# Performance work log

Hardware: AMD Instinct MI355X
Metric: run time of the kernel (lower is better)

Reference implementation:

```python
import jax, jax.numpy as jnp
import numpy as np

DIM = 512
NUM_HEADS = 8
HEAD_DIM = DIM // NUM_HEADS
EPS = 1e-6


def setup_inputs() -> dict:
    key = jax.random.key(0)
    k_x, k_qkv, k_out, k_b = jax.random.split(key, 4)
    B, N = 8, 4096
    x = jax.random.normal(k_x, (B, N, DIM), dtype=jnp.float32)
    # nn.Linear weights stored as [out_features, in_features]; we keep [in, out] for x @ W
    s_qkv = 1.0 / np.sqrt(DIM)
    W_qkv = jax.random.uniform(k_qkv, (DIM, 3 * DIM), minval=-s_qkv, maxval=s_qkv, dtype=jnp.float32)
    W_out = jax.random.uniform(k_out, (DIM, DIM), minval=-s_qkv, maxval=s_qkv, dtype=jnp.float32)
    b_out = jax.random.uniform(k_b, (DIM,), minval=-s_qkv, maxval=s_qkv, dtype=jnp.float32)
    return {"x": x, "W_qkv": W_qkv, "W_out": W_out, "b_out": b_out}


def _feature_map(x):
    # elu(x) + 1
    return jax.nn.elu(x) + 1.0


def reference(x, W_qkv, W_out, b_out):
    B, N, C = x.shape
    H, D = NUM_HEADS, HEAD_DIM
    qkv = x @ W_qkv                              # [B, N, 3C]
    qkv = qkv.reshape(B, N, 3, H, D).transpose(2, 0, 3, 1, 4)  # [3, B, H, N, D]
    q, k, v = qkv[0], qkv[1], qkv[2]
    q_phi = _feature_map(q)                      # [B, H, N, D]
    k_phi = _feature_map(k)
    KV = jnp.einsum('bhnd,bhne->bhde', k_phi, v)  # [B, H, D, D]
    K_sum = k_phi.sum(axis=2)                     # [B, H, D]
    denom = jnp.einsum('bhnd,bhd->bhn', q_phi, K_sum)[..., None] + EPS  # [B, H, N, 1]
    out = jnp.einsum('bhnd,bhde->bhne', q_phi, KV) / denom              # [B, H, N, D]
    out = out.transpose(0, 2, 1, 3).reshape(B, N, C)
    return out @ W_out + b_out
```

## Files before the change

### kernel.cpp

```cpp
#include <hip/hip_runtime.h>
#include <stdint.h>

typedef float    f32x4 __attribute__((ext_vector_type(4)));
typedef short    s16x8 __attribute__((ext_vector_type(8)));
typedef short    s16x4 __attribute__((ext_vector_type(4)));
typedef unsigned short u16;
typedef uint32_t u32;

#define DEVINL __device__ __forceinline__

DEVINL float bf2f(u16 u) { union { u32 i; float f; } x; x.i = ((u32)u) << 16; return x.f; }
DEVINL u16 f2bf(float f) {
  union { float f; u32 i; } x; x.f = f;
  u32 i = x.i;
  return (u16)((i + 0x7FFFu + ((i >> 16) & 1u)) >> 16);
}

DEVINL void gload16(const void* g, void* l) {
  __builtin_amdgcn_global_load_lds((const __attribute__((address_space(1))) void*)g,
                                   (__attribute__((address_space(3))) void*)l,
                                   16, 0, 0);
}

__global__ __launch_bounds__(256) void k_prep(const float* __restrict__ x,
                                              u16* __restrict__ xb,
                                              const float* __restrict__ Wqkv,
                                              u16* __restrict__ wqkvt,
                                              const float* __restrict__ Wout,
                                              u16* __restrict__ woutt) {
  __shared__ __align__(16) float t[64][65];
  int b = blockIdx.x;
  int tid = threadIdx.x;
  if (b < 2048) {
    const int n8 = 2097152;
    int stride = 2048 * 256;
    for (int i = b * 256 + tid; i < n8; i += stride) {
      const f32x4* p = (const f32x4*)(x + (size_t)i * 8);
      f32x4 a = p[0], c = p[1];
      s16x8 o;
      o[0] = (short)f2bf(a[0]); o[1] = (short)f2bf(a[1]);
      o[2] = (short)f2bf(a[2]); o[3] = (short)f2bf(a[3]);
      o[4] = (short)f2bf(c[0]); o[5] = (short)f2bf(c[1]);
      o[6] = (short)f2bf(c[2]); o[7] = (short)f2bf(c[3]);
      *(s16x8*)(xb + (size_t)i * 8) = o;
    }
    return;
  }
  const float* W; u16* Wt; int K, N, tb;
  if (b < 2048 + 192) { W = Wqkv; Wt = wqkvt; K = 512; N = 1536; tb = b - 2048; }
  else               { W = Wout; Wt = woutt; K = 512; N = 512;  tb = b - 2240; }
  int nb = N >> 6;
  int tn = tb % nb, tk = tb / nb;
  int n0 = tn << 6, k0 = tk << 6;
  int cr = tid >> 4, cc = (tid & 15) << 2;
#pragma unroll
  for (int i = 0; i < 4; i++) {
    int r = cr + (i << 4);
    f32x4 v = *(const f32x4*)(W + (size_t)(k0 + r) * N + n0 + cc);
    t[r][cc] = v[0]; t[r][cc + 1] = v[1]; t[r][cc + 2] = v[2]; t[r][cc + 3] = v[3];
  }
  __syncthreads();
#pragma unroll
  for (int i = 0; i < 4; i++) {
    int nn = cr + (i << 4);
    s16x4 o;
    o[0] = (short)f2bf(t[cc    ][nn]);
    o[1] = (short)f2bf(t[cc + 1][nn]);
    o[2] = (short)f2bf(t[cc + 2][nn]);
    o[3] = (short)f2bf(t[cc + 3][nn]);
    *(s16x4*)(Wt + (size_t)(n0 + nn) * K + k0 + cc) = o;
  }
}

__global__ __launch_bounds__(256, 2) void k_g1(
    const u16* __restrict__ A, const u16* __restrict__ Bt,
    u16* __restrict__ qph, u16* __restrict__ kphT, u16* __restrict__ vT) {
  __shared__ __align__(16) u16 lsA[3][128 * 32];
  __shared__ __align__(16) u16 lsB[3][256 * 32];
  const int nbn = 6;
  int nwg = gridDim.x, bx = blockIdx.x;
  int o = (bx & 7) * (nwg >> 3) + (bx >> 3);
  int bm = o / nbn, bn = o % nbn;
  int m0 = bm << 7, n0 = bn << 8;
  int tid = threadIdx.x, w = tid >> 6, lane = tid & 63;
  int lnlo = lane & 15, lnhi = lane >> 4;

  if ((bx >> 8) & 1) __builtin_amdgcn_s_sleep(30);

  const u16* gAp[2]; int lda[2];
#pragma unroll
  for (int i = 0; i < 2; i++) {
    int c = tid + i * 256, row = c >> 2, ch = c & 3;
    gAp[i] = A + (size_t)(m0 + row) * 512 + (ch ^ ((row >> 1) & 3)) * 8;
    lda[i] = c * 8;
  }
  const u16* gBp[4]; int ldb[4];
#pragma unroll
  for (int i = 0; i < 4; i++) {
    int c = tid + i * 256, row = c >> 2, ch = c & 3;
    gBp[i] = Bt + (size_t)(n0 + row) * 512 + (ch ^ ((row >> 1) & 3)) * 8;
    ldb[i] = c * 8;
  }
  int offA[8], offB[4];
#pragma unroll
  for (int f = 0; f < 8; f++) { int r = f * 16 + lnlo;          offA[f] = r * 32 + (lnhi ^ ((r >> 1) & 3)) * 8; }
#pragma unroll
  for (int f = 0; f < 4; f++) { int r = w * 64 + f * 16 + lnlo; offB[f] = r * 32 + (lnhi ^ ((r >> 1) & 3)) * 8; }

  f32x4 acc[8][4] = {};

#pragma unroll
  for (int tt = 0; tt < 2; tt++) {
#pragma unroll
    for (int i = 0; i < 2; i++) gload16(gAp[i] + tt * 32, &lsA[tt][lda[i]]);
#pragma unroll
    for (int i = 0; i < 4; i++) gload16(gBp[i] + tt * 32, &lsB[tt][ldb[i]]);
  }
  asm volatile("s_waitcnt vmcnt(6)" ::: "memory");
  __builtin_amdgcn_s_barrier();

#pragma unroll
  for (int t = 0; t < 16; t++) {
    int buf = t % 3;
    const u16* La = &lsA[buf][0];
    const u16* Lb = &lsB[buf][0];
    int k2 = (t + 2) * 32, b2 = (t + 2) % 3;

    s16x8 bf[4], af[4];
#pragma unroll
    for (int f = 0; f < 4; f++) bf[f] = *(const s16x8*)(Lb + offB[f]);
#pragma unroll
    for (int f = 0; f < 4; f++) af[f] = *(const s16x8*)(La + offA[f]);
    if (t < 14) {
#pragma unroll
      for (int i = 0; i < 2; i++) gload16(gAp[i] + k2, &lsA[b2][lda[i]]);
    }
    __builtin_amdgcn_s_barrier();
    __builtin_amdgcn_s_setprio(1);
#pragma unroll
    for (int mf = 0; mf < 4; mf++)
#pragma unroll
      for (int nf = 0; nf < 4; nf++)
        acc[mf][nf] = __builtin_amdgcn_mfma_f32_16x16x32_bf16(af[mf], bf[nf], acc[mf][nf], 0, 0, 0);
    __builtin_amdgcn_s_setprio(0);
    __builtin_amdgcn_s_barrier();

    s16x8 af2[4];
#pragma unroll
    for (int f = 0; f < 4; f++) af2[f] = *(const s16x8*)(La + offA[4 + f]);
    if (t < 14) {
#pragma unroll
      for (int i = 0; i < 4; i++) gload16(gBp[i] + k2, &lsB[b2][ldb[i]]);
    }
    __builtin_amdgcn_s_barrier();
    __builtin_amdgcn_s_setprio(1);
#pragma unroll
    for (int mf = 0; mf < 4; mf++)
#pragma unroll
      for (int nf = 0; nf < 4; nf++)
        acc[4 + mf][nf] = __builtin_amdgcn_mfma_f32_16x16x32_bf16(af2[mf], bf[nf], acc[4 + mf][nf], 0, 0, 0);
    __builtin_amdgcn_s_setprio(0);
    if (t <= 13)      asm volatile("s_waitcnt vmcnt(6)" ::: "memory");
    else if (t == 14) asm volatile("s_waitcnt vmcnt(0)" ::: "memory");
    if (t < 15) __builtin_amdgcn_s_barrier();
  }

  int gnB = n0 + w * 64;
  int sec = n0 >> 9;
  if (sec == 0) {
#pragma unroll
    for (int mf = 0; mf < 8; mf++) {
#pragma unroll
      for (int nf = 0; nf < 4; nf++) {
        int col = gnB + nf * 16 + lnlo;
        int hh = (col >> 6) & 7;
        int dd = col & 63;
#pragma unroll
        for (int r = 0; r < 4; r++) {
          int rowm = m0 + mf * 16 + lnhi * 4 + r;
          float val = acc[mf][nf][r];
          val = (val > 0.f) ? (val + 1.f) : __expf(val);
          int bidx = rowm >> 12, tok = rowm & 4095;
          qph[(((size_t)(bidx * 8 + hh) * 4096 + tok) << 6) + dd] = f2bf(val);
        }
      }
    }
  } else {
    u16* dstT = (sec == 1) ? kphT : vT;
    bool isphi = (sec == 1);
#pragma unroll
    for (int mf = 0; mf < 8; mf++) {
      int rowm = m0 + mf * 16 + lnhi * 4;
      int bidx = rowm >> 12, tok = rowm & 4095;
#pragma unroll
      for (int nf = 0; nf < 4; nf++) {
        int col = gnB + nf * 16 + lnlo;
        int hh = (col >> 6) & 7;
        int dd = col & 63;
        s16x4 o4;
#pragma unroll
        for (int r = 0; r < 4; r++) {
          float val = acc[mf][nf][r];
          if (isphi) val = (val > 0.f) ? (val + 1.f) : __expf(val);
          o4[r] = (short)f2bf(val);
        }
        *(s16x4*)&dstT[((size_t)(bidx * 8 + hh) * 64 + dd) * 4096 + tok] = o4;
      }
    }
  }
}

template <int EPI>
__global__ __launch_bounds__(512, 1) void k_gemm(
    const u16* __restrict__ A, const u16* __restrict__ Bt,
    int nbn,
    u16* __restrict__ qph, u16* __restrict__ kphT, u16* __restrict__ vT,
    float* __restrict__ out, const float* __restrict__ bias) {
  __shared__ __align__(16) u16 lsA[3][256 * 32];
  __shared__ __align__(16) u16 lsB[3][256 * 32];

  int nwg = gridDim.x;
  int bx = blockIdx.x;
  int o = (bx & 7) * (nwg >> 3) + (bx >> 3);
  int bm = o / nbn, bn = o % nbn;
  int m0 = bm << 8, n0 = bn << 8;
  int tid = threadIdx.x;
  int w = tid >> 6, lane = tid & 63;
  int lnlo = lane & 15, lnhi = lane >> 4;
  int wr = w >> 2, wc = w & 3;

  const u16* gAp[2]; const u16* gBp[2]; int ldst[2];
#pragma unroll
  for (int i = 0; i < 2; i++) {
    int c = tid + i * 512;
    int row = c >> 2, ch = c & 3;
    int gch = ch ^ ((row >> 1) & 3);
    gAp[i] = A + (size_t)(m0 + row) * 512 + gch * 8;
    gBp[i] = Bt + (size_t)(n0 + row) * 512 + gch * 8;
    ldst[i] = c * 8;
  }

  int offA[8], offB[4];
#pragma unroll
  for (int f = 0; f < 8; f++) {
    int r = wr * 128 + f * 16 + lnlo;
    offA[f] = r * 32 + (lnhi ^ ((r >> 1) & 3)) * 8;
  }
#pragma unroll
  for (int f = 0; f < 4; f++) {
    int r = wc * 64 + f * 16 + lnlo;
    offB[f] = r * 32 + (lnhi ^ ((r >> 1) & 3)) * 8;
  }

  f32x4 acc[8][4] = {};

#pragma unroll
  for (int i = 0; i < 2; i++) gload16(gAp[i], &lsA[0][ldst[i]]);
#pragma unroll
  for (int i = 0; i < 2; i++) gload16(gBp[i], &lsB[0][ldst[i]]);
#pragma unroll
  for (int i = 0; i < 2; i++) gload16(gAp[i] + 32, &lsA[1][ldst[i]]);
#pragma unroll
  for (int i = 0; i < 2; i++) gload16(gBp[i] + 32, &lsB[1][ldst[i]]);
  asm volatile("s_waitcnt vmcnt(4)" ::: "memory");
  __builtin_amdgcn_s_barrier();

#pragma unroll
  for (int t = 0; t < 16; t++) {
    int buf = t % 3;
    const u16* La = &lsA[buf][0];
    const u16* Lb = &lsB[buf][0];
    int k2 = (t + 2) * 32;
    int b2 = (t + 2) % 3;

    s16x8 bf[4], af[4];
#pragma unroll
    for (int f = 0; f < 4; f++) bf[f] = *(const s16x8*)(Lb + offB[f]);
#pragma unroll
    for (int f = 0; f < 4; f++) af[f] = *(const s16x8*)(La + offA[f]);
    if (t < 14) {
#pragma unroll
      for (int i = 0; i < 2; i++) gload16(gAp[i] + k2, &lsA[b2][ldst[i]]);
    }
    __builtin_amdgcn_s_barrier();
    __builtin_amdgcn_s_setprio(1);
#pragma unroll
    for (int mf = 0; mf < 4; mf++)
#pragma unroll
      for (int nf = 0; nf < 4; nf++)
        acc[mf][nf] = __builtin_amdgcn_mfma_f32_16x16x32_bf16(af[mf], bf[nf], acc[mf][nf], 0, 0, 0);
    __builtin_amdgcn_s_setprio(0);
    __builtin_amdgcn_s_barrier();

    s16x8 af2[4];
#pragma unroll
    for (int f = 0; f < 4; f++) af2[f] = *(const s16x8*)(La + offA[4 + f]);
    if (t < 14) {
#pragma unroll
      for (int i = 0; i < 2; i++) gload16(gBp[i] + k2, &lsB[b2][ldst[i]]);
    }
    __builtin_amdgcn_s_barrier();
    __builtin_amdgcn_s_setprio(1);
#pragma unroll
    for (int mf = 0; mf < 4; mf++)
#pragma unroll
      for (int nf = 0; nf < 4; nf++)
        acc[4 + mf][nf] = __builtin_amdgcn_mfma_f32_16x16x32_bf16(af2[mf], bf[nf], acc[4 + mf][nf], 0, 0, 0);
    __builtin_amdgcn_s_setprio(0);
    if (t <= 13)      asm volatile("s_waitcnt vmcnt(4)" ::: "memory");
    else if (t == 14) asm volatile("s_waitcnt vmcnt(0)" ::: "memory");
    if (t < 15) __builtin_amdgcn_s_barrier();
  }

  int gmB = m0 + wr * 128;
  int gnB = n0 + wc * 64;
#pragma unroll
  for (int mf = 0; mf < 8; mf++) {
#pragma unroll
    for (int nf = 0; nf < 4; nf++) {
      int col = gnB + nf * 16 + lnlo;
      float bv = bias[col];
#pragma unroll
      for (int r = 0; r < 4; r++) {
        int rowm = gmB + mf * 16 + lnhi * 4 + r;
        out[(size_t)rowm * 512 + col] = acc[mf][nf][r] + bv;
      }
    }
  }
}

__global__ __launch_bounds__(256, 2) void k_kv(const u16* __restrict__ kphT,
                                               const u16* __restrict__ vT,
                                               float* __restrict__ kvpart,
                                               float* __restrict__ kspart) {
  __shared__ __align__(16) u16 lsK[64 * 256];
  __shared__ __align__(16) u16 lsV[64 * 256];
  __shared__ float red[4][64];
  int bx = blockIdx.x;
  int bh = bx >> 4, ck = bx & 15;
  int tid = threadIdx.x, w = tid >> 6, lane = tid & 63;
  int lnlo = lane & 15, lnhi = lane >> 4;
  size_t gbase = (size_t)bh * 64 * 4096 + ck * 256;

#pragma unroll
  for (int i = 0; i < 8; i++) {
    int c = tid + i * 256;
    int row = c >> 5, ch = c & 31;
    int gch = ch ^ (row & 31);
    gload16(kphT + gbase + (size_t)row * 4096 + gch * 8, &lsK[c * 8]);
  }
#pragma unroll
  for (int i = 0; i < 8; i++) {
    int c = tid + i * 256;
    int row = c >> 5, ch = c & 31;
    int gch = ch ^ (row & 31);
    gload16(vT + gbase + (size_t)row * 4096 + gch * 8, &lsV[c * 8]);
  }
  asm volatile("s_waitcnt vmcnt(0)" ::: "memory");
  __builtin_amdgcn_s_barrier();

  f32x4 acc[4] = {{0.f, 0.f, 0.f, 0.f}, {0.f, 0.f, 0.f, 0.f},
                  {0.f, 0.f, 0.f, 0.f}, {0.f, 0.f, 0.f, 0.f}};
  int rb = w * 16 + lnlo;
#pragma unroll
  for (int kk = 0; kk < 8; kk++) {
    s16x8 bfr = *(const s16x8*)&lsV[rb * 256 + ((kk * 4 + lnhi) ^ (rb & 31)) * 8];
#pragma unroll
    for (int mf = 0; mf < 4; mf++) {
      int ra = mf * 16 + lnlo;
      s16x8 af = *(const s16x8*)&lsK[ra * 256 + ((kk * 4 + lnhi) ^ (ra & 31)) * 8];
      acc[mf] = __builtin_amdgcn_mfma_f32_16x16x32_bf16(af, bfr, acc[mf], 0, 0, 0);
    }
  }

  {
    int d = tid & 63, q = tid >> 6;
    float s = 0.f;
#pragma unroll
    for (int j = 0; j < 8; j++) {
      s16x8 v8 = *(const s16x8*)&lsK[d * 256 + (q * 8 + j) * 8];
#pragma unroll
      for (int e = 0; e < 8; e++) s += bf2f((u16)v8[e]);
    }
    red[q][d] = s;
  }
  __syncthreads();

  size_t pb = (size_t)(bh * 16 + ck) * 4096;
#pragma unroll
  for (int mf = 0; mf < 4; mf++)
#pragma unroll
    for (int r = 0; r < 4; r++)
      kvpart[pb + (size_t)(mf * 16 + lnhi * 4 + r) * 64 + (w * 16 + lnlo)] = acc[mf][r];
  if (tid < 64)
    kspart[(size_t)(bh * 16 + ck) * 64 + tid] =
        red[0][tid] + red[1][tid] + red[2][tid] + red[3][tid];
}

__global__ __launch_bounds__(256) void k_kvred(const float* __restrict__ kvpart,
                                               const float* __restrict__ kspart,
                                               u16* __restrict__ kvt_sw,
                                               float* __restrict__ ksum) {
  int bh = blockIdx.x;
  int tid = threadIdx.x;
  int e = tid >> 2, d0 = (tid & 3) * 16;
  size_t pb = (size_t)bh * 16 * 4096;
#pragma unroll
  for (int dd = 0; dd < 16; dd++) {
    int d = d0 + dd;
    float s = 0.f;
#pragma unroll
    for (int c = 0; c < 16; c++) s += kvpart[pb + (size_t)c * 4096 + d * 64 + e];
    int chs = (d >> 3) ^ (e & 7);
    kvt_sw[((size_t)bh * 64 + e) * 64 + chs * 8 + (d & 7)] = f2bf(s);
  }
  if (tid < 64) {
    float s = 0.f;
#pragma unroll
    for (int c = 0; c < 16; c++) s += kspart[(size_t)bh * 1024 + c * 64 + tid];
    ksum[bh * 64 + tid] = s;
  }
}

__global__ __launch_bounds__(256, 2) void k_attnout(const u16* __restrict__ qphi,
                                                    const u16* __restrict__ kvt_sw,
                                                    const float* __restrict__ ksum,
                                                    u16* __restrict__ y) {
  __shared__ __align__(16) u16 qa[256 * 64];
  __shared__ __align__(16) u16 bb[64 * 64];
  __shared__ float ksl[64];
  __shared__ float rdnl[256];
  int bx = blockIdx.x;
  int bh = bx >> 4, tch = bx & 15;
  int b = bh >> 3, hh = bh & 7;
  int tid = threadIdx.x, w = tid >> 6, lane = tid & 63;
  int lnlo = lane & 15, lnhi = lane >> 4;
  size_t qbase = ((size_t)bh * 4096 + tch * 256) * 64;

#pragma unroll
  for (int i = 0; i < 8; i++) {
    int c = i * 256 + tid;
    int row = c >> 3, ch = c & 7;
    int gcol = (ch ^ (row & 7)) << 3;
    gload16(qphi + qbase + (size_t)row * 64 + gcol, &qa[c * 8]);
  }
#pragma unroll
  for (int i = 0; i < 2; i++) {
    int c = i * 256 + tid;
    gload16(kvt_sw + (size_t)bh * 4096 + c * 8, &bb[c * 8]);
  }
  if (tid < 64) ksl[tid] = ksum[bh * 64 + tid];
  __syncthreads();

  {
    float den = 0.f;
#pragma unroll
    for (int ch = 0; ch < 8; ch++) {
      s16x8 v8 = *(const s16x8*)&qa[tid * 64 + ((ch ^ (tid & 7)) << 3)];
#pragma unroll
      for (int j = 0; j < 8; j++) den += bf2f((u16)v8[j]) * ksl[ch * 8 + j];
    }
    rdnl[tid] = 1.f / (den + 1e-6f);
  }
  __syncthreads();

  f32x4 acc[4][4] = {};
#pragma unroll
  for (int kk = 0; kk < 2; kk++) {
    s16x8 af[4], bfr[4];
#pragma unroll
    for (int f = 0; f < 4; f++) {
      int ra = w * 64 + f * 16 + lnlo;
      int ca = (kk * 4 + lnhi) ^ (ra & 7);
      af[f] = *(const s16x8*)&qa[ra * 64 + ca * 8];
      int rb = f * 16 + lnlo;
      int cb = (kk * 4 + lnhi) ^ (rb & 7);
      bfr[f] = *(const s16x8*)&bb[rb * 64 + cb * 8];
    }
#pragma unroll
    for (int mf = 0; mf < 4; mf++)
#pragma unroll
      for (int nf = 0; nf < 4; nf++)
        acc[mf][nf] = __builtin_amdgcn_mfma_f32_16x16x32_bf16(af[mf], bfr[nf], acc[mf][nf], 0, 0, 0);
  }

  size_t yrow0 = (size_t)b * 4096 + tch * 256;
#pragma unroll
  for (int mf = 0; mf < 4; mf++) {
#pragma unroll
    for (int nf = 0; nf < 4; nf++) {
      int e = nf * 16 + lnlo;
#pragma unroll
      for (int r = 0; r < 4; r++) {
        int tl = w * 64 + mf * 16 + lnhi * 4 + r;
        float val = acc[mf][nf][r] * rdnl[tl];
        y[(yrow0 + tl) * 512 + hh * 64 + e] = f2bf(val);
      }
    }
  }
}

#define OFF_XB     ((size_t)0)
#define OFF_WQKVT  ((size_t)33554432)
#define OFF_WOUTT  ((size_t)35127296)
#define OFF_QPHI   ((size_t)35651584)
#define OFF_KPHI   ((size_t)69206016)
#define OFF_VBUF   ((size_t)102760448)
#define OFF_KVPART ((size_t)136314880)
#define OFF_KSPART ((size_t)153092096)
#define OFF_KVT    ((size_t)153354240)
#define OFF_KSUM   ((size_t)153878528)

extern "C" void kernel_launch(void* const* d_in, const int* in_sizes, int n_in,
                              void* d_out, int out_size, void* d_ws, size_t ws_size,
                              hipStream_t stream) {
  const float* x    = (const float*)d_in[0];
  const float* Wqkv = (const float*)d_in[1];
  const float* Wout = (const float*)d_in[2];
  const float* bout = (const float*)d_in[3];
  float* out = (float*)d_out;
  char* ws = (char*)d_ws;

  u16* xb     = (u16*)(ws + OFF_XB);
  u16* y      = (u16*)(ws + OFF_XB);
  u16* wqkvt  = (u16*)(ws + OFF_WQKVT);
  u16* woutt  = (u16*)(ws + OFF_WOUTT);
  u16* qphi   = (u16*)(ws + OFF_QPHI);
  u16* kphT   = (u16*)(ws + OFF_KPHI);
  u16* vT     = (u16*)(ws + OFF_VBUF);
  float* kvpart = (float*)(ws + OFF_KVPART);
  float* kspart = (float*)(ws + OFF_KSPART);
  u16* kvt_sw = (u16*)(ws + OFF_KVT);
  float* ksum = (float*)(ws + OFF_KSUM);

  k_prep<<<2304, 256, 0, stream>>>(x, xb, Wqkv, wqkvt, Wout, woutt);

  k_g1<<<1536, 256, 0, stream>>>(xb, wqkvt, qphi, kphT, vT);
  k_kv<<<64 * 16, 256, 0, stream>>>(kphT, vT, kvpart, kspart);
  k_kvred<<<64, 256, 0, stream>>>(kvpart, kspart, kvt_sw, ksum);
  k_attnout<<<64 * 16, 256, 0, stream>>>(qphi, kvt_sw, ksum, y);
  k_gemm<1><<<256, 512, 0, stream>>>(y, woutt, 2, nullptr, nullptr, nullptr, out, bout);
}
```

Measured before the change: 160.8 us.

## Fold KV into output projection per batch and fuse attention-out into final GEMM

Precomputes per-batch W2 = blockdiag(KV_h) · W_out so the output becomes (q_phi scaled by 1/denom) @ W2 + bias. The separate attention-out kernel, its bf16 intermediate y, and the KV reduce kernel are removed, and the row normalization is applied while staging A tiles into LDS in the final GEMM. The QKV GEMM also moves from the 128x256 tile with 256 threads to the 256x256 tile with 512 threads. In exchange there is an extra small GEMM per batch and head to build W2, the A tiles go through registers instead of direct-to-LDS loads, and there is an extra bf16 rounding of W2.

Measured after the change: 153.6 us (median of 2 runs). 4.5% less time.

```diff
diff --git a/kernel.cpp b/kernel.cpp
--- a/kernel.cpp
+++ b/kernel.cpp
@@ -72,153 +72,12 @@
   }
 }
 
-__global__ __launch_bounds__(256, 2) void k_g1(
+__global__ __launch_bounds__(512, 1) void k_gemm1(
     const u16* __restrict__ A, const u16* __restrict__ Bt,
     u16* __restrict__ qph, u16* __restrict__ kphT, u16* __restrict__ vT) {
-  __shared__ __align__(16) u16 lsA[3][128 * 32];
+  __shared__ __align__(16) u16 lsA[3][256 * 32];
   __shared__ __align__(16) u16 lsB[3][256 * 32];
   const int nbn = 6;
-  int nwg = gridDim.x, bx = blockIdx.x;
-  int o = (bx & 7) * (nwg >> 3) + (bx >> 3);
-  int bm = o / nbn, bn = o % nbn;
-  int m0 = bm << 7, n0 = bn << 8;
-  int tid = threadIdx.x, w = tid >> 6, lane = tid & 63;
-  int lnlo = lane & 15, lnhi = lane >> 4;
-
-  if ((bx >> 8) & 1) __builtin_amdgcn_s_sleep(30);
-
-  const u16* gAp[2]; int lda[2];
-#pragma unroll
-  for (int i = 0; i < 2; i++) {
-    int c = tid + i * 256, row = c >> 2, ch = c & 3;
-    gAp[i] = A + (size_t)(m0 + row) * 512 + (ch ^ ((row >> 1) & 3)) * 8;
-    lda[i] = c * 8;
-  }
-  const u16* gBp[4]; int ldb[4];
-#pragma unroll
-  for (int i = 0; i < 4; i++) {
-    int c = tid + i * 256, row = c >> 2, ch = c & 3;
-    gBp[i] = Bt + (size_t)(n0 + row) * 512 + (ch ^ ((row >> 1) & 3)) * 8;
-    ldb[i] = c * 8;
-  }
-  int offA[8], offB[4];
-#pragma unroll
-  for (int f = 0; f < 8; f++) { int r = f * 16 + lnlo;          offA[f] = r * 32 + (lnhi ^ ((r >> 1) & 3)) * 8; }
-#pragma unroll
-  for (int f = 0; f < 4; f++) { int r = w * 64 + f * 16 + lnlo; offB[f] = r * 32 + (lnhi ^ ((r >> 1) & 3)) * 8; }
-
-  f32x4 acc[8][4] = {};
-
-#pragma unroll
-  for (int tt = 0; tt < 2; tt++) {
-#pragma unroll
-    for (int i = 0; i < 2; i++) gload16(gAp[i] + tt * 32, &lsA[tt][lda[i]]);
-#pragma unroll
-    for (int i = 0; i < 4; i++) gload16(gBp[i] + tt * 32, &lsB[tt][ldb[i]]);
-  }
-  asm volatile("s_waitcnt vmcnt(6)" ::: "memory");
-  __builtin_amdgcn_s_barrier();
-
-#pragma unroll
-  for (int t = 0; t < 16; t++) {
-    int buf = t % 3;
-    const u16* La = &lsA[buf][0];
-    const u16* Lb = &lsB[buf][0];
-    int k2 = (t + 2) * 32, b2 = (t + 2) % 3;
-
-    s16x8 bf[4], af[4];
-#pragma unroll
-    for (int f = 0; f < 4; f++) bf[f] = *(const s16x8*)(Lb + offB[f]);
-#pragma unroll
-    for (int f = 0; f < 4; f++) af[f] = *(const s16x8*)(La + offA[f]);
-    if (t < 14) {
-#pragma unroll
-      for (int i = 0; i < 2; i++) gload16(gAp[i] + k2, &lsA[b2][lda[i]]);
-    }
-    __builtin_amdgcn_s_barrier();
-    __builtin_amdgcn_s_setprio(1);
-#pragma unroll
-    for (int mf = 0; mf < 4; mf++)
-#pragma unroll
-      for (int nf = 0; nf < 4; nf++)
-        acc[mf][nf] = __builtin_amdgcn_mfma_f32_16x16x32_bf16(af[mf], bf[nf], acc[mf][nf], 0, 0, 0);
-    __builtin_amdgcn_s_setprio(0);
-    __builtin_amdgcn_s_barrier();
-
-    s16x8 af2[4];
-#pragma unroll
-    for (int f = 0; f < 4; f++) af2[f] = *(const s16x8*)(La + offA[4 + f]);
-    if (t < 14) {
-#pragma unroll
-      for (int i = 0; i < 4; i++) gload16(gBp[i] + k2, &lsB[b2][ldb[i]]);
-    }
-    __builtin_amdgcn_s_barrier();
-    __builtin_amdgcn_s_setprio(1);
-#pragma unroll
-    for (int mf = 0; mf < 4; mf++)
-#pragma unroll
-      for (int nf = 0; nf < 4; nf++)
-        acc[4 + mf][nf] = __builtin_amdgcn_mfma_f32_16x16x32_bf16(af2[mf], bf[nf], acc[4 + mf][nf], 0, 0, 0);
-    __builtin_amdgcn_s_setprio(0);
-    if (t <= 13)      asm volatile("s_waitcnt vmcnt(6)" ::: "memory");
-    else if (t == 14) asm volatile("s_waitcnt vmcnt(0)" ::: "memory");
-    if (t < 15) __builtin_amdgcn_s_barrier();
-  }
-
-  int gnB = n0 + w * 64;
-  int sec = n0 >> 9;
-  if (sec == 0) {
-#pragma unroll
-    for (int mf = 0; mf < 8; mf++) {
-#pragma unroll
-      for (int nf = 0; nf < 4; nf++) {
-        int col = gnB + nf * 16 + lnlo;
-        int hh = (col >> 6) & 7;
-        int dd = col & 63;
-#pragma unroll
-        for (int r = 0; r < 4; r++) {
-          int rowm = m0 + mf * 16 + lnhi * 4 + r;
-          float val = acc[mf][nf][r];
-          val = (val > 0.f) ? (val + 1.f) : __expf(val);
-          int bidx = rowm >> 12, tok = rowm & 4095;
-          qph[(((size_t)(bidx * 8 + hh) * 4096 + tok) << 6) + dd] = f2bf(val);
-        }
-      }
-    }
-  } else {
-    u16* dstT = (sec == 1) ? kphT : vT;
-    bool isphi = (sec == 1);
-#pragma unroll
-    for (int mf = 0; mf < 8; mf++) {
-      int rowm = m0 + mf * 16 + lnhi * 4;
-      int bidx = rowm >> 12, tok = rowm & 4095;
-#pragma unroll
-      for (int nf = 0; nf < 4; nf++) {
-        int col = gnB + nf * 16 + lnlo;
-        int hh = (col >> 6) & 7;
-        int dd = col & 63;
-        s16x4 o4;
-#pragma unroll
-        for (int r = 0; r < 4; r++) {
-          float val = acc[mf][nf][r];
-          if (isphi) val = (val > 0.f) ? (val + 1.f) : __expf(val);
-          o4[r] = (short)f2bf(val);
-        }
-        *(s16x4*)&dstT[((size_t)(bidx * 8 + hh) * 64 + dd) * 4096 + tok] = o4;
-      }
-    }
-  }
-}
-
-template <int EPI>
-__global__ __launch_bounds__(512, 1) void k_gemm(
-    const u16* __restrict__ A, const u16* __restrict__ Bt,
-    int nbn,
-    u16* __restrict__ qph, u16* __restrict__ kphT, u16* __restrict__ vT,
-    float* __restrict__ out, const float* __restrict__ bias) {
-  __shared__ __align__(16) u16 lsA[3][256 * 32];
-  __shared__ __align__(16) u16 lsB[3][256 * 32];
-
   int nwg = gridDim.x;
   int bx = blockIdx.x;
   int o = (bx & 7) * (nwg >> 3) + (bx >> 3);
@@ -239,7 +98,6 @@
     gBp[i] = Bt + (size_t)(n0 + row) * 512 + gch * 8;
     ldst[i] = c * 8;
   }
-
   int offA[8], offB[4];
 #pragma unroll
   for (int f = 0; f < 8; f++) {
@@ -314,16 +172,45 @@
 
   int gmB = m0 + wr * 128;
   int gnB = n0 + wc * 64;
-#pragma unroll
-  for (int mf = 0; mf < 8; mf++) {
-#pragma unroll
-    for (int nf = 0; nf < 4; nf++) {
-      int col = gnB + nf * 16 + lnlo;
-      float bv = bias[col];
-#pragma unroll
-      for (int r = 0; r < 4; r++) {
-        int rowm = gmB + mf * 16 + lnhi * 4 + r;
-        out[(size_t)rowm * 512 + col] = acc[mf][nf][r] + bv;
+  int sec = n0 >> 9;
+  if (sec == 0) {
+#pragma unroll
+    for (int mf = 0; mf < 8; mf++) {
+#pragma unroll
+      for (int nf = 0; nf < 4; nf++) {
+        int col = gnB + nf * 16 + lnlo;
+        int hh = (col >> 6) & 7;
+        int dd = col & 63;
+#pragma unroll
+        for (int r = 0; r < 4; r++) {
+          int rowm = gmB + mf * 16 + lnhi * 4 + r;
+          float val = acc[mf][nf][r];
+          val = (val > 0.f) ? (val + 1.f) : __expf(val);
+          int bidx = rowm >> 12, tok = rowm & 4095;
+          qph[(((size_t)(bidx * 8 + hh) * 4096 + tok) << 6) + dd] = f2bf(val);
+        }
+      }
+    }
+  } else {
+    u16* dstT = (sec == 1) ? kphT : vT;
+    bool isphi = (sec == 1);
+#pragma unroll
+    for (int mf = 0; mf < 8; mf++) {
+      int rowm = gmB + mf * 16 + lnhi * 4;
+      int bidx = rowm >> 12, tok = rowm & 4095;
+#pragma unroll
+      for (int nf = 0; nf < 4; nf++) {
+        int col = gnB + nf * 16 + lnlo;
+        int hh = (col >> 6) & 7;
+        int dd = col & 63;
+        s16x4 o4;
+#pragma unroll
+        for (int r = 0; r < 4; r++) {
+          float val = acc[mf][nf][r];
+          if (isphi) val = (val > 0.f) ? (val + 1.f) : __expf(val);
+          o4[r] = (short)f2bf(val);
+        }
+        *(s16x4*)&dstT[((size_t)(bidx * 8 + hh) * 64 + dd) * 4096 + tok] = o4;
       }
     }
   }
@@ -397,110 +284,231 @@
         red[0][tid] + red[1][tid] + red[2][tid] + red[3][tid];
 }
 
-__global__ __launch_bounds__(256) void k_kvred(const float* __restrict__ kvpart,
-                                               const float* __restrict__ kspart,
-                                               u16* __restrict__ kvt_sw,
-                                               float* __restrict__ ksum) {
-  int bh = blockIdx.x;
-  int tid = threadIdx.x;
-  int e = tid >> 2, d0 = (tid & 3) * 16;
-  size_t pb = (size_t)bh * 16 * 4096;
-#pragma unroll
-  for (int dd = 0; dd < 16; dd++) {
-    int d = d0 + dd;
-    float s = 0.f;
-#pragma unroll
-    for (int c = 0; c < 16; c++) s += kvpart[pb + (size_t)c * 4096 + d * 64 + e];
-    int chs = (d >> 3) ^ (e & 7);
-    kvt_sw[((size_t)bh * 64 + e) * 64 + chs * 8 + (d & 7)] = f2bf(s);
-  }
-  if (tid < 64) {
-    float s = 0.f;
-#pragma unroll
-    for (int c = 0; c < 16; c++) s += kspart[(size_t)bh * 1024 + c * 64 + tid];
-    ksum[bh * 64 + tid] = s;
-  }
-}
-
-__global__ __launch_bounds__(256, 2) void k_attnout(const u16* __restrict__ qphi,
-                                                    const u16* __restrict__ kvt_sw,
-                                                    const float* __restrict__ ksum,
-                                                    u16* __restrict__ y) {
-  __shared__ __align__(16) u16 qa[256 * 64];
-  __shared__ __align__(16) u16 bb[64 * 64];
-  __shared__ float ksl[64];
-  __shared__ float rdnl[256];
-  int bx = blockIdx.x;
-  int bh = bx >> 4, tch = bx & 15;
-  int b = bh >> 3, hh = bh & 7;
+__global__ __launch_bounds__(256) void k_w2(const float* __restrict__ kvpart,
+                                            const float* __restrict__ kspart,
+                                            const u16* __restrict__ woutt,
+                                            const u16* __restrict__ qphi,
+                                            u16* __restrict__ w2t,
+                                            float* __restrict__ rdng) {
+  __shared__ __align__(16) u16 kvls[64 * 64];
+  __shared__ float ksumv[64];
+  int blk = blockIdx.x, tid = threadIdx.x;
+  if (blk < 64) {
+    int bh = blk, b = bh >> 3, h = bh & 7;
+    int w = tid >> 6, lane = tid & 63, lnlo = lane & 15, lnhi = lane >> 4;
+    int d = tid >> 2, e0 = (tid & 3) << 4;
+    size_t pb = (size_t)bh * 16 * 4096;
+    f32x4 s0 = {}, s1 = {}, s2 = {}, s3 = {};
+    for (int c = 0; c < 16; c++) {
+      const float* p = kvpart + pb + (size_t)c * 4096 + d * 64 + e0;
+      s0 += *(const f32x4*)(p);
+      s1 += *(const f32x4*)(p + 4);
+      s2 += *(const f32x4*)(p + 8);
+      s3 += *(const f32x4*)(p + 12);
+    }
+    s16x8 o0, o1;
+#pragma unroll
+    for (int j = 0; j < 4; j++) {
+      o0[j] = (short)f2bf(s0[j]); o0[4 + j] = (short)f2bf(s1[j]);
+      o1[j] = (short)f2bf(s2[j]); o1[4 + j] = (short)f2bf(s3[j]);
+    }
+    int ch0 = e0 >> 3;
+    *(s16x8*)&kvls[d * 64 + (ch0 ^ (d & 7)) * 8] = o0;
+    *(s16x8*)&kvls[d * 64 + ((ch0 + 1) ^ (d & 7)) * 8] = o1;
+    __syncthreads();
+    f32x4 acc[4][8] = {};
+#pragma unroll
+    for (int kk = 0; kk < 2; kk++) {
+      s16x8 af[4], bfr[8];
+#pragma unroll
+      for (int mf = 0; mf < 4; mf++) {
+        int r = mf * 16 + lnlo;
+        af[mf] = *(const s16x8*)&kvls[r * 64 + ((kk * 4 + lnhi) ^ (r & 7)) * 8];
+      }
+#pragma unroll
+      for (int nf = 0; nf < 8; nf++) {
+        int n = w * 128 + nf * 16 + lnlo;
+        bfr[nf] = *(const s16x8*)&woutt[(size_t)n * 512 + h * 64 + (kk * 4 + lnhi) * 8];
+      }
+#pragma unroll
+      for (int mf = 0; mf < 4; mf++)
+#pragma unroll
+        for (int nf = 0; nf < 8; nf++)
+          acc[mf][nf] = __builtin_amdgcn_mfma_f32_16x16x32_bf16(af[mf], bfr[nf], acc[mf][nf], 0, 0, 0);
+    }
+#pragma unroll
+    for (int mf = 0; mf < 4; mf++)
+#pragma unroll
+      for (int nf = 0; nf < 8; nf++) {
+        int n = w * 128 + nf * 16 + lnlo;
+        s16x4 o4;
+#pragma unroll
+        for (int r = 0; r < 4; r++) o4[r] = (short)f2bf(acc[mf][nf][r]);
+        *(s16x4*)&w2t[(size_t)b * 262144 + (size_t)n * 512 + h * 64 + mf * 16 + lnhi * 4] = o4;
+      }
+  } else {
+    int blk2 = blk - 64;
+    int bh = blk2 >> 3, tch = blk2 & 7;
+    if (tid < 64) {
+      float s = 0.f;
+#pragma unroll
+      for (int c = 0; c < 16; c++) s += kspart[(size_t)bh * 1024 + c * 64 + tid];
+      ksumv[tid] = s;
+    }
+    __syncthreads();
+#pragma unroll
+    for (int tt = 0; tt < 2; tt++) {
+      int tok = tch * 512 + tid * 2 + tt;
+      const u16* qp = qphi + ((size_t)bh * 4096 + tok) * 64;
+      float den = 0.f;
+#pragma unroll
+      for (int cch = 0; cch < 8; cch++) {
+        s16x8 v8 = *(const s16x8*)(qp + cch * 8);
+        f32x4 k0 = *(const f32x4*)&ksumv[cch * 8];
+        f32x4 k1 = *(const f32x4*)&ksumv[cch * 8 + 4];
+#pragma unroll
+        for (int j = 0; j < 4; j++) den += bf2f((u16)v8[j]) * k0[j];
+#pragma unroll
+        for (int j = 0; j < 4; j++) den += bf2f((u16)v8[4 + j]) * k1[j];
+      }
+      rdng[(size_t)bh * 4096 + tok] = 1.f / (den + 1e-6f);
+    }
+  }
+}
+
+__global__ __launch_bounds__(512, 1) void k_out(
+    const u16* __restrict__ qphi, const u16* __restrict__ w2t,
+    const float* __restrict__ rdng, const float* __restrict__ bias,
+    float* __restrict__ out) {
+  __shared__ __align__(16) u16 lsA[3][256 * 32];
+  __shared__ __align__(16) u16 lsB[3][256 * 32];
+  int nwg = gridDim.x, bx = blockIdx.x;
+  int o = (bx & 7) * (nwg >> 3) + (bx >> 3);
+  int bm = o >> 1, bn = o & 1;
+  int m0 = bm << 8, n0 = bn << 8;
+  int b = m0 >> 12;
   int tid = threadIdx.x, w = tid >> 6, lane = tid & 63;
   int lnlo = lane & 15, lnhi = lane >> 4;
-  size_t qbase = ((size_t)bh * 4096 + tch * 256) * 64;
-
-#pragma unroll
-  for (int i = 0; i < 8; i++) {
-    int c = i * 256 + tid;
-    int row = c >> 3, ch = c & 7;
-    int gcol = (ch ^ (row & 7)) << 3;
-    gload16(qphi + qbase + (size_t)row * 64 + gcol, &qa[c * 8]);
-  }
+  int wr = w >> 2, wc = w & 3;
+
+  int ldst[2];
+  const u16* qb_[2]; const u16* gB_[2]; const float* rb_[2];
 #pragma unroll
   for (int i = 0; i < 2; i++) {
-    int c = i * 256 + tid;
-    gload16(kvt_sw + (size_t)bh * 4096 + c * 8, &bb[c * 8]);
-  }
-  if (tid < 64) ksl[tid] = ksum[bh * 64 + tid];
-  __syncthreads();
-
-  {
-    float den = 0.f;
-#pragma unroll
-    for (int ch = 0; ch < 8; ch++) {
-      s16x8 v8 = *(const s16x8*)&qa[tid * 64 + ((ch ^ (tid & 7)) << 3)];
-#pragma unroll
-      for (int j = 0; j < 8; j++) den += bf2f((u16)v8[j]) * ksl[ch * 8 + j];
-    }
-    rdnl[tid] = 1.f / (den + 1e-6f);
-  }
-  __syncthreads();
-
-  f32x4 acc[4][4] = {};
-#pragma unroll
-  for (int kk = 0; kk < 2; kk++) {
-    s16x8 af[4], bfr[4];
-#pragma unroll
-    for (int f = 0; f < 4; f++) {
-      int ra = w * 64 + f * 16 + lnlo;
-      int ca = (kk * 4 + lnhi) ^ (ra & 7);
-      af[f] = *(const s16x8*)&qa[ra * 64 + ca * 8];
-      int rb = f * 16 + lnlo;
-      int cb = (kk * 4 + lnhi) ^ (rb & 7);
-      bfr[f] = *(const s16x8*)&bb[rb * 64 + cb * 8];
-    }
+    int c = tid + i * 512, row = c >> 2, ch = c & 3;
+    int gch = ch ^ ((row >> 1) & 3);
+    int tok = (m0 + row) & 4095;
+    qb_[i] = qphi + ((size_t)(b * 8) * 4096 + tok) * 64 + gch * 8;
+    rb_[i] = rdng + (size_t)(b * 8) * 4096 + tok;
+    gB_[i] = w2t + (size_t)b * 262144 + (size_t)(n0 + row) * 512 + gch * 8;
+    ldst[i] = c * 8;
+  }
+  int offA[8], offB[4];
+#pragma unroll
+  for (int f = 0; f < 8; f++) {
+    int r = wr * 128 + f * 16 + lnlo;
+    offA[f] = r * 32 + (lnhi ^ ((r >> 1) & 3)) * 8;
+  }
+#pragma unroll
+  for (int f = 0; f < 4; f++) {
+    int r = wc * 64 + f * 16 + lnlo;
+    offB[f] = r * 32 + (lnhi ^ ((r >> 1) & 3)) * 8;
+  }
+
+  f32x4 acc[8][4] = {};
+  s16x8 ar[2]; float rr[2];
+
+  auto loadA = [&](int t) {
+#pragma unroll
+    for (int i = 0; i < 2; i++) {
+      ar[i] = *(const s16x8*)(qb_[i] + (size_t)(t >> 1) * 262144 + (t & 1) * 32);
+      rr[i] = rb_[i][(size_t)(t >> 1) * 4096];
+    }
+  };
+  auto writeA = [&](int buf) {
+#pragma unroll
+    for (int i = 0; i < 2; i++) {
+      s16x8 oo;
+#pragma unroll
+      for (int j = 0; j < 8; j++) oo[j] = (short)f2bf(bf2f((u16)ar[i][j]) * rr[i]);
+      *(s16x8*)&lsA[buf][ldst[i]] = oo;
+    }
+  };
+  auto stageB = [&](int t) {
+    int buf = t % 3;
+#pragma unroll
+    for (int i = 0; i < 2; i++) gload16(gB_[i] + t * 32, &lsB[buf][ldst[i]]);
+  };
+
+  loadA(0); writeA(0);
+  loadA(1); writeA(1);
+  stageB(0); stageB(1);
+  asm volatile("s_waitcnt lgkmcnt(0)" ::: "memory");
+  asm volatile("s_waitcnt vmcnt(2)" ::: "memory");
+  __builtin_amdgcn_s_barrier();
+
+#pragma unroll
+  for (int t = 0; t < 16; t++) {
+    int buf = t % 3;
+    const u16* La = &lsA[buf][0];
+    const u16* Lb = &lsB[buf][0];
+
+    s16x8 bf[4], af[4];
+#pragma unroll
+    for (int f = 0; f < 4; f++) bf[f] = *(const s16x8*)(Lb + offB[f]);
+#pragma unroll
+    for (int f = 0; f < 4; f++) af[f] = *(const s16x8*)(La + offA[f]);
+    if (t < 14) loadA(t + 2);
+    __builtin_amdgcn_s_barrier();
+    __builtin_amdgcn_s_setprio(1);
 #pragma unroll
     for (int mf = 0; mf < 4; mf++)
 #pragma unroll
       for (int nf = 0; nf < 4; nf++)
-        acc[mf][nf] = __builtin_amdgcn_mfma_f32_16x16x32_bf16(af[mf], bfr[nf], acc[mf][nf], 0, 0, 0);
-  }
-
-  size_t yrow0 = (size_t)b * 4096 + tch * 256;
-#pragma unroll
-  for (int mf = 0; mf < 4; mf++) {
+        acc[mf][nf] = __builtin_amdgcn_mfma_f32_16x16x32_bf16(af[mf], bf[nf], acc[mf][nf], 0, 0, 0);
+    __builtin_amdgcn_s_setprio(0);
+    __builtin_amdgcn_s_barrier();
+
+    s16x8 af2[4];
+#pragma unroll
+    for (int f = 0; f < 4; f++) af2[f] = *(const s16x8*)(La + offA[4 + f]);
+    if (t < 14) stageB(t + 2);
+    __builtin_amdgcn_s_barrier();
+    __builtin_amdgcn_s_setprio(1);
+#pragma unroll
+    for (int mf = 0; mf < 4; mf++)
+#pragma unroll
+      for (int nf = 0; nf < 4; nf++)
+        acc[4 + mf][nf] = __builtin_amdgcn_mfma_f32_16x16x32_bf16(af2[mf], bf[nf], acc[4 + mf][nf], 0, 0, 0);
+    __builtin_amdgcn_s_setprio(0);
+    if (t < 14) writeA((t + 2) % 3);
+    if (t == 14) asm volatile("s_waitcnt vmcnt(0)" ::: "memory");
+    if (t < 15) {
+      asm volatile("s_waitcnt lgkmcnt(0)" ::: "memory");
+      __builtin_amdgcn_s_barrier();
+    }
+  }
+
+  int gmB = m0 + wr * 128;
+  int gnB = n0 + wc * 64;
+#pragma unroll
+  for (int mf = 0; mf < 8; mf++) {
 #pragma unroll
     for (int nf = 0; nf < 4; nf++) {
-      int e = nf * 16 + lnlo;
+      int col = gnB + nf * 16 + lnlo;
+      float bv = bias[col];
 #pragma unroll
       for (int r = 0; r < 4; r++) {
-        int tl = w * 64 + mf * 16 + lnhi * 4 + r;
-        float val = acc[mf][nf][r] * rdnl[tl];
-        y[(yrow0 + tl) * 512 + hh * 64 + e] = f2bf(val);
+        int rowm = gmB + mf * 16 + lnhi * 4 + r;
+        out[(size_t)rowm * 512 + col] = acc[mf][nf][r] + bv;
       }
     }
   }
 }
 
 #define OFF_XB     ((size_t)0)
+#define OFF_W2T    ((size_t)0)
+#define OFF_RDN    ((size_t)4194304)
 #define OFF_WQKVT  ((size_t)33554432)
 #define OFF_WOUTT  ((size_t)35127296)
 #define OFF_QPHI   ((size_t)35651584)
@@ -508,8 +516,6 @@
 #define OFF_VBUF   ((size_t)102760448)
 #define OFF_KVPART ((size_t)136314880)
 #define OFF_KSPART ((size_t)153092096)
-#define OFF_KVT    ((size_t)153354240)
-#define OFF_KSUM   ((size_t)153878528)
 
 extern "C" void kernel_launch(void* const* d_in, const int* in_sizes, int n_in,
                               void* d_out, int out_size, void* d_ws, size_t ws_size,
@@ -522,7 +528,8 @@
   char* ws = (char*)d_ws;
 
   u16* xb     = (u16*)(ws + OFF_XB);
-  u16* y      = (u16*)(ws + OFF_XB);
+  u16* w2t    = (u16*)(ws + OFF_W2T);
+  float* rdng = (float*)(ws + OFF_RDN);
   u16* wqkvt  = (u16*)(ws + OFF_WQKVT);
   u16* woutt  = (u16*)(ws + OFF_WOUTT);
   u16* qphi   = (u16*)(ws + OFF_QPHI);
@@ -530,14 +537,10 @@
   u16* vT     = (u16*)(ws + OFF_VBUF);
   float* kvpart = (float*)(ws + OFF_KVPART);
   float* kspart = (float*)(ws + OFF_KSPART);
-  u16* kvt_sw = (u16*)(ws + OFF_KVT);
-  float* ksum = (float*)(ws + OFF_KSUM);
 
   k_prep<<<2304, 256, 0, stream>>>(x, xb, Wqkv, wqkvt, Wout, woutt);
-
-  k_g1<<<1536, 256, 0, stream>>>(xb, wqkvt, qphi, kphT, vT);
-  k_kv<<<64 * 16, 256, 0, stream>>>(kphT, vT, kvpart, kspart);
-  k_kvred<<<64, 256, 0, stream>>>(kvpart, kspart, kvt_sw, ksum);
-  k_attnout<<<64 * 16, 256, 0, stream>>>(qphi, kvt_sw, ksum, y);
-  k_gemm<1><<<256, 512, 0, stream>>>(y, woutt, 2, nullptr, nullptr, nullptr, out, bout);
-}
+  k_gemm1<<<768, 512, 0, stream>>>(xb, wqkvt, qphi, kphT, vT);
+  k_kv<<<1024, 256, 0, stream>>>(kphT, vT, kvpart, kspart);
+  k_w2<<<576, 256, 0, stream>>>(kvpart, kspart, woutt, qphi, w2t, rdng);
+  k_out<<<256, 512, 0, stream>>>(qphi, w2t, rdng, bout, out);
+}
```
